# Performance work log

Hardware: AMD Instinct MI355X
Metric: run time of the kernel (lower is better)

## Reference

```python
import jax, jax.numpy as jnp
import numpy as np

N = 50000
E = 800000
DIM_IN = 128
DIM_H = 16
HEADS = 8
DIM_OUT = 16
NEG_SLOPE = 0.2


def setup_inputs() -> dict:
    key = jax.random.key(0)
    ks = jax.random.split(key, 12)
    def glorot(k, shape):
        fan_in = shape[0]
        return jax.random.normal(k, shape, dtype=jnp.float32) / np.sqrt(fan_in)
    x = jax.random.normal(ks[0], (N, DIM_IN), dtype=jnp.float32)
    edge_index = jax.random.randint(ks[1], (2, E), 0, N, dtype=jnp.int64)
    # layer 1: GATv2Conv(dim_in, dim_h, heads=8)
    Wl1 = glorot(ks[2], (DIM_IN, HEADS * DIM_H))
    Wr1 = glorot(ks[3], (DIM_IN, HEADS * DIM_H))
    att1 = glorot(ks[4], (HEADS, DIM_H))
    bias1 = jnp.zeros((HEADS * DIM_H,), dtype=jnp.float32)
    # layer 2: GATv2Conv(dim_h*heads, dim_out, heads=1)
    Wl2 = glorot(ks[5], (HEADS * DIM_H, DIM_OUT))
    Wr2 = glorot(ks[6], (HEADS * DIM_H, DIM_OUT))
    att2 = glorot(ks[7], (1, DIM_OUT))
    bias2 = jnp.zeros((DIM_OUT,), dtype=jnp.float32)
    return {"x": x, "edge_index": edge_index, "Wl1": Wl1, "Wr1": Wr1,
            "att1": att1, "bias1": bias1, "Wl2": Wl2, "Wr2": Wr2,
            "att2": att2, "bias2": bias2}


def gatv2_layer(x, src, dst, Wl, Wr, att, bias, n_nodes, heads, ch):
    # x: [N, F_in]; src/dst: [Etot] (self-loops included)
    xl = (x @ Wl).reshape(n_nodes, heads, ch)  # source transform
    xr = (x @ Wr).reshape(n_nodes, heads, ch)  # target transform
    e = jax.nn.leaky_relu(xl[src] + xr[dst], NEG_SLOPE)      # [Etot, H, C]
    logits = jnp.einsum('ehc,hc->eh', e, att)                # [Etot, H]
    # segment softmax over incoming edges of each target node
    m = jax.ops.segment_max(logits, dst, num_segments=n_nodes)
    a = jnp.exp(logits - m[dst])
    denom = jax.ops.segment_sum(a, dst, num_segments=n_nodes)
    alpha = a / denom[dst]                                   # [Etot, H]
    out = jax.ops.segment_sum(xl[src] * alpha[:, :, None], dst,
                              num_segments=n_nodes)          # [N, H, C]
    return out.reshape(n_nodes, heads * ch) + bias


def reference(x, edge_index, Wl1, Wr1, att1, bias1, Wl2, Wr2, att2, bias2):
    # PyG GATv2Conv adds self-loops by default
    loops = jnp.arange(N, dtype=edge_index.dtype)
    src = jnp.concatenate([edge_index[0], loops])
    dst = jnp.concatenate([edge_index[1], loops])
    # dropout is identity in eval mode
    h = gatv2_layer(x, src, dst, Wl1, Wr1, att1, bias1, N, HEADS, DIM_H)
    h = jax.nn.elu(h)
    h = gatv2_layer(h, src, dst, Wl2, Wr2, att2, bias2, N, 1, DIM_OUT)
    return h, jax.nn.log_softmax(h, axis=1)
```

## Files before the change

kernel.cpp:

```cpp
#include <hip/hip_runtime.h>
#include <hip/hip_bf16.h>
#include <math.h>

#define NN 50000
#define EE 800000
#define DIN 128
#define HEADS 8
#define DH 16
#define DOUT 16
#define NEG 0.2f
#define GM 32
#define GB ((NN + GM - 1) / GM)
#define NB ((NN + 255) / 256)
#define ABLK ((EE / 4 + 255) / 256)
#define NPART 8
#define RANGE (NN / NPART)
#define RB 1563
#define SCATB 64
#define BUCKCAP 110000
#define PAD 64

typedef __attribute__((ext_vector_type(8))) short bf16x8;
typedef __attribute__((ext_vector_type(4))) float f32x4;
typedef __attribute__((ext_vector_type(4))) int i32x4;

__device__ __forceinline__ unsigned pack2bf(float a, float b) {
    union { __hip_bfloat162 h; unsigned u; } c;
    c.h = __float22bfloat162_rn(make_float2(a, b));
    return c.u;
}
__device__ __forceinline__ unsigned short f2bf(float v) {
    union { __hip_bfloat16 h; unsigned short u; } c;
    c.h = __float2bfloat16(v);
    return c.u;
}
__device__ __forceinline__ float bflo(unsigned u) { return __uint_as_float(u << 16); }
__device__ __forceinline__ float bfhi(unsigned u) { return __uint_as_float(u & 0xffff0000u); }

__global__ __launch_bounds__(256) void init_wcvt(int* __restrict__ cnt,
                                                 unsigned* __restrict__ bhead,
                                                 const float* __restrict__ Wl,
                                                 const float* __restrict__ Wr,
                                                 unsigned short* __restrict__ Wb,
                                                 const float* __restrict__ Wl2,
                                                 const float* __restrict__ Wr2,
                                                 unsigned short* __restrict__ Wb2) {
    int b = blockIdx.x, t = threadIdx.x;
    if (b == 0 && t < 8) bhead[t] = 0;
    if (b < NB) {
        int i = b * 256 + t;
        if (i < NN) cnt[i] = 1;
    } else if (b < NB + 128) {
        int i = (b - NB) * 256 + t;
        int n = i >> 7, k = i & 127;
        float v = (n < 128) ? Wl[k * 128 + n] : Wr[k * 128 + (n - 128)];
        Wb[i] = f2bf(v);
    } else {
        int i = (b - NB - 128) * 256 + t;
        int n = i >> 7, k = i & 127;
        float v = (n < 16) ? Wl2[k * 16 + n] : Wr2[k * 16 + (n - 16)];
        Wb2[i] = f2bf(v);
    }
}

__global__ __launch_bounds__(256) void fill_gemm1(const int* __restrict__ ei,
                                                  unsigned* __restrict__ bhead,
                                                  unsigned* __restrict__ bucket,
                                                  const float* __restrict__ x,
                                                  const unsigned short* __restrict__ Wb,
                                                  unsigned short* __restrict__ xlb,
                                                  float* __restrict__ xr) {
    __shared__ unsigned short As[GM][136];
    int t = threadIdx.x;
    if (blockIdx.x < ABLK) {
        unsigned* lrec = (unsigned*)&As[0][0];
        unsigned* lcnt = lrec + 1024;
        unsigned* loff = lcnt + 8;
        unsigned* lpos = loff + 8;
        unsigned* gbase = lpos + 8;
        int i = blockIdx.x * 256 + t;
        bool valid = i < EE / 4;
        i32x4 ss, dd;
        unsigned bb[4];
        if (valid) {
            ss = __builtin_nontemporal_load(((const i32x4*)ei) + i);
            dd = __builtin_nontemporal_load(((const i32x4*)(ei + EE)) + i);
        }
        if (t < 8) { lcnt[t] = 0; lpos[t] = 0; }
        __syncthreads();
        if (valid) {
#pragma unroll
            for (int e = 0; e < 4; ++e) {
                bb[e] = (unsigned)dd[e] / RANGE;
                atomicAdd(&lcnt[bb[e]], 1u);
            }
        }
        __syncthreads();
        if (t == 0) {
            unsigned run = 0;
#pragma unroll
            for (int q = 0; q < 8; ++q) { loff[q] = run; run += lcnt[q]; }
        }
        if (t < 8 && lcnt[t] > 0) gbase[t] = atomicAdd(&bhead[t], lcnt[t]);
        __syncthreads();
        if (valid) {
#pragma unroll
            for (int e = 0; e < 4; ++e) {
                unsigned p = atomicAdd(&lpos[bb[e]], 1u);
                lrec[loff[bb[e]] + p] = ((unsigned)ss[e] << 16) | (unsigned)dd[e];
            }
        }
        __syncthreads();
        unsigned total = loff[7] + lcnt[7];
        for (unsigned j = t; j < total; j += 256) {
            unsigned q = 0;
            while (q < 7 && j >= loff[q + 1]) ++q;
            bucket[(size_t)q * BUCKCAP + gbase[q] + (j - loff[q])] = lrec[j];
        }
        return;
    }
    int n0 = (blockIdx.x - ABLK) * GM;
    {
        int row = t >> 3, seg = t & 7;
        int nsrc = n0 + row < NN ? n0 + row : NN - 1;
        const f32x4* xp = (const f32x4*)(x + (size_t)nsrc * DIN + 16 * seg);
        f32x4 v0 = __builtin_nontemporal_load(xp);
        f32x4 v1 = __builtin_nontemporal_load(xp + 1);
        f32x4 v2 = __builtin_nontemporal_load(xp + 2);
        f32x4 v3 = __builtin_nontemporal_load(xp + 3);
        uint4 p0 = make_uint4(pack2bf(v0[0], v0[1]), pack2bf(v0[2], v0[3]),
                              pack2bf(v1[0], v1[1]), pack2bf(v1[2], v1[3]));
        uint4 p1 = make_uint4(pack2bf(v2[0], v2[1]), pack2bf(v2[2], v2[3]),
                              pack2bf(v3[0], v3[1]), pack2bf(v3[2], v3[3]));
        *(uint4*)&As[row][16 * seg]     = p0;
        *(uint4*)&As[row][16 * seg + 8] = p1;
    }
    __syncthreads();
    int lane = t & 63, w = t >> 6;
    int m = lane & 15, quad = lane >> 4;
    f32x4 acc[2][4];
#pragma unroll
    for (int mt = 0; mt < 2; ++mt)
#pragma unroll
        for (int nt = 0; nt < 4; ++nt) acc[mt][nt] = (f32x4){0.f, 0.f, 0.f, 0.f};
#pragma unroll
    for (int ks = 0; ks < 4; ++ks) {
        int k = 32 * ks + 8 * quad;
        bf16x8 a0 = *(const bf16x8*)&As[m][k];
        bf16x8 a1 = *(const bf16x8*)&As[16 + m][k];
#pragma unroll
        for (int nt = 0; nt < 4; ++nt) {
            int n = 64 * w + 16 * nt + m;
            bf16x8 b = *(const bf16x8*)(Wb + (size_t)n * 128 + k);
            acc[0][nt] = __builtin_amdgcn_mfma_f32_16x16x32_bf16(a0, b, acc[0][nt], 0, 0, 0);
            acc[1][nt] = __builtin_amdgcn_mfma_f32_16x16x32_bf16(a1, b, acc[1][nt], 0, 0, 0);
        }
    }
#pragma unroll
    for (int mt = 0; mt < 2; ++mt) {
#pragma unroll
        for (int nt = 0; nt < 4; ++nt) {
            int col = 64 * w + 16 * nt + m;
            int rbase = n0 + 16 * mt + 4 * quad;
            if (col < 128) {
#pragma unroll
                for (int r = 0; r < 4; ++r) {
                    int row = rbase + r;
                    if (row < NN) xlb[(size_t)row * DIN + col] = f2bf(acc[mt][nt][r]);
                }
            } else {
#pragma unroll
                for (int r = 0; r < 4; ++r) {
                    int row = rbase + r;
                    if (row < NN) xr[(size_t)row * DIN + (col - 128)] = acc[mt][nt][r];
                }
            }
        }
    }
}

__global__ __launch_bounds__(256) void scatter_b(const unsigned* __restrict__ bucket,
                                                 const unsigned* __restrict__ bhead,
                                                 int* __restrict__ cnt,
                                                 unsigned short* __restrict__ esrcPad) {
    int r = blockIdx.x & 7;
    int g = blockIdx.x >> 3;
    int t = threadIdx.x;
    if (g == 0) {
        for (int dq = t; dq < RANGE; dq += 256) {
            int d = r * RANGE + dq;
            esrcPad[(size_t)d * PAD] = (unsigned short)d;
        }
    }
    unsigned n = bhead[r];
    for (unsigned i = (unsigned)g * 256 + t; i < n; i += SCATB * 256) {
        unsigned rec = __builtin_nontemporal_load(bucket + (size_t)r * BUCKCAP + i);
        unsigned s = rec >> 16, d = rec & 0xffffu;
        int p = atomicAdd(&cnt[d], 1);
        esrcPad[(size_t)d * PAD + p] = (unsigned short)s;
    }
}

__global__ __launch_bounds__(256) void l1_fused(const unsigned short* __restrict__ esrcPad,
                                                const int* __restrict__ cnt,
                                                const unsigned short* __restrict__ xlb,
                                                const float* __restrict__ xr,
                                                const float* __restrict__ att,
                                                const float* __restrict__ bias,
                                                unsigned short* __restrict__ hb) {
    int r = blockIdx.x & 7;
    int dq = (blockIdx.x >> 3) * 4 + (threadIdx.x >> 6);
    if (dq >= RANGE) return;
    int d = r * RANGE + dq;
    int lane = threadIdx.x & 63;
    int quarter = lane >> 4;
    int q16 = lane & 15;
    int rs = d * PAD;
    int re = rs + cnt[d];
    int last = re - 1;
    float4 xr0 = ((const float4*)(xr + (size_t)d * DIN))[2 * q16];
    float4 xr1 = ((const float4*)(xr + (size_t)d * DIN))[2 * q16 + 1];
    float4 at0 = ((const float4*)att)[2 * q16];
    float4 at1 = ((const float4*)att)[2 * q16 + 1];
    float4 a0 = make_float4(0.f, 0.f, 0.f, 0.f);
    float4 a1 = make_float4(0.f, 0.f, 0.f, 0.f);
    float l = 0.f;
    int slot = rs + quarter;
    int c0 = slot < last ? slot : last;
    int s0 = esrcPad[c0];
    int c1 = slot + 4 < last ? slot + 4 : last;
    int s1 = esrcPad[c1];
    uint4 row = ((const uint4*)(xlb + (size_t)s0 * DIN))[q16];
    for (; slot < re; slot += 4) {
        uint4 cur = row;
        int c2 = slot + 8 < last ? slot + 8 : last;
        int s2 = esrcPad[c2];
        row = ((const uint4*)(xlb + (size_t)s1 * DIN))[q16];
        s1 = s2;
        float f0 = bflo(cur.x), f1 = bfhi(cur.x);
        float f2 = bflo(cur.y), f3 = bfhi(cur.y);
        float f4 = bflo(cur.z), f5 = bfhi(cur.z);
        float f6 = bflo(cur.w), f7 = bfhi(cur.w);
        float v0 = f0 + xr0.x; v0 = fmaxf(v0, NEG * v0);
        float v1 = f1 + xr0.y; v1 = fmaxf(v1, NEG * v1);
        float v2 = f2 + xr0.z; v2 = fmaxf(v2, NEG * v2);
        float v3 = f3 + xr0.w; v3 = fmaxf(v3, NEG * v3);
        float v4 = f4 + xr1.x; v4 = fmaxf(v4, NEG * v4);
        float v5 = f5 + xr1.y; v5 = fmaxf(v5, NEG * v5);
        float v6 = f6 + xr1.z; v6 = fmaxf(v6, NEG * v6);
        float v7 = f7 + xr1.w; v7 = fmaxf(v7, NEG * v7);
        float w = at0.x * v0 + at0.y * v1 + at0.z * v2 + at0.w * v3
                + at1.x * v4 + at1.y * v5 + at1.z * v6 + at1.w * v7;
        w += __shfl_xor(w, 1);
        float p = __expf(w);
        a0.x += p * f0; a0.y += p * f1; a0.z += p * f2; a0.w += p * f3;
        a1.x += p * f4; a1.y += p * f5; a1.z += p * f6; a1.w += p * f7;
        l += p;
    }
#pragma unroll
    for (int off = 16; off < 64; off <<= 1) {
        a0.x += __shfl_xor(a0.x, off); a0.y += __shfl_xor(a0.y, off);
        a0.z += __shfl_xor(a0.z, off); a0.w += __shfl_xor(a0.w, off);
        a1.x += __shfl_xor(a1.x, off); a1.y += __shfl_xor(a1.y, off);
        a1.z += __shfl_xor(a1.z, off); a1.w += __shfl_xor(a1.w, off);
        l += __shfl_xor(l, off);
    }
    if (quarter == 0) {
        float inv = 1.f / l;
        float4 b0 = ((const float4*)bias)[2 * q16];
        float4 b1 = ((const float4*)bias)[2 * q16 + 1];
        float4 o0, o1;
        o0.x = a0.x * inv + b0.x; o0.x = o0.x > 0.f ? o0.x : expm1f(o0.x);
        o0.y = a0.y * inv + b0.y; o0.y = o0.y > 0.f ? o0.y : expm1f(o0.y);
        o0.z = a0.z * inv + b0.z; o0.z = o0.z > 0.f ? o0.z : expm1f(o0.z);
        o0.w = a0.w * inv + b0.w; o0.w = o0.w > 0.f ? o0.w : expm1f(o0.w);
        o1.x = a1.x * inv + b1.x; o1.x = o1.x > 0.f ? o1.x : expm1f(o1.x);
        o1.y = a1.y * inv + b1.y; o1.y = o1.y > 0.f ? o1.y : expm1f(o1.y);
        o1.z = a1.z * inv + b1.z; o1.z = o1.z > 0.f ? o1.z : expm1f(o1.z);
        o1.w = a1.w * inv + b1.w; o1.w = o1.w > 0.f ? o1.w : expm1f(o1.w);
        uint4 pk = make_uint4(pack2bf(o0.x, o0.y), pack2bf(o0.z, o0.w),
                              pack2bf(o1.x, o1.y), pack2bf(o1.z, o1.w));
        ((uint4*)(hb + (size_t)d * DIN))[q16] = pk;
    }
}

__global__ __launch_bounds__(256) void gemm2(const unsigned short* __restrict__ hb,
                                             const unsigned short* __restrict__ Wb2,
                                             float* __restrict__ xl2, float* __restrict__ xr2) {
    __shared__ unsigned short As[GM][136];
    int t = threadIdx.x;
    int n0 = blockIdx.x * GM;
    {
        int row = t >> 3, s8 = t & 7;
        int nsrc = n0 + row < NN ? n0 + row : NN - 1;
        const uint4* src = (const uint4*)(hb + (size_t)nsrc * DIN);
        *(uint4*)&As[row][8 * s8]      = src[s8];
        *(uint4*)&As[row][8 * s8 + 64] = src[s8 + 8];
    }
    __syncthreads();
    int lane = t & 63, w = t >> 6;
    int m = lane & 15, quad = lane >> 4;
    int mt = w & 1, nt = w >> 1;
    f32x4 acc = (f32x4){0.f, 0.f, 0.f, 0.f};
#pragma unroll
    for (int ks = 0; ks < 4; ++ks) {
        int k = 32 * ks + 8 * quad;
        bf16x8 a = *(const bf16x8*)&As[16 * mt + m][k];
        bf16x8 b = *(const bf16x8*)(Wb2 + (size_t)(16 * nt + m) * 128 + k);
        acc = __builtin_amdgcn_mfma_f32_16x16x32_bf16(a, b, acc, 0, 0, 0);
    }
    float* __restrict__ dst = (nt == 0) ? xl2 : xr2;
#pragma unroll
    for (int r = 0; r < 4; ++r) {
        int node = n0 + 16 * mt + 4 * quad + r;
        if (node < NN) dst[(size_t)node * DOUT + m] = acc[r];
    }
}

__global__ __launch_bounds__(256) void l2_fused(const unsigned short* __restrict__ esrcPad,
                                                const int* __restrict__ cnt,
                                                const float* __restrict__ xl,
                                                const float* __restrict__ xr,
                                                const float* __restrict__ att,
                                                const float* __restrict__ bias,
                                                float* __restrict__ out) {
    int r = blockIdx.x & 7;
    int dq = (blockIdx.x >> 3) * 4 + (threadIdx.x >> 6);
    if (dq >= RANGE) return;
    int d = r * RANGE + dq;
    int lane = threadIdx.x & 63;
    int sl = lane >> 2;
    int q = lane & 3;
    int rs = d * PAD;
    int re = rs + cnt[d];
    int last = re - 1;
    float4 xrq = ((const float4*)(xr + (size_t)d * DOUT))[q];
    float4 atq = ((const float4*)att)[q];
    float4 acc = make_float4(0.f, 0.f, 0.f, 0.f);
    float l = 0.f;
    int slot = rs + sl;
    int c0 = slot < last ? slot : last;
    int s0 = esrcPad[c0];
    for (; slot < re; slot += 16) {
        int c1 = slot + 16 < last ? slot + 16 : last;
        int s1 = esrcPad[c1];
        float4 cur = ((const float4*)(xl + (size_t)s0 * DOUT))[q];
        s0 = s1;
        float v0 = cur.x + xrq.x; v0 = fmaxf(v0, NEG * v0);
        float v1 = cur.y + xrq.y; v1 = fmaxf(v1, NEG * v1);
        float v2 = cur.z + xrq.z; v2 = fmaxf(v2, NEG * v2);
        float v3 = cur.w + xrq.w; v3 = fmaxf(v3, NEG * v3);
        float w = atq.x * v0 + atq.y * v1 + atq.z * v2 + atq.w * v3;
        w += __shfl_xor(w, 1);
        w += __shfl_xor(w, 2);
        float p = __expf(w);
        acc.x += p * cur.x; acc.y += p * cur.y;
        acc.z += p * cur.z; acc.w += p * cur.w;
        l += p;
    }
#pragma unroll
    for (int off = 4; off < 64; off <<= 1) {
        acc.x += __shfl_xor(acc.x, off);
        acc.y += __shfl_xor(acc.y, off);
        acc.z += __shfl_xor(acc.z, off);
        acc.w += __shfl_xor(acc.w, off);
        l += __shfl_xor(l, off);
    }
    float inv = 1.f / l;
    float4 b = ((const float4*)bias)[q];
    float4 v;
    v.x = acc.x * inv + b.x; v.y = acc.y * inv + b.y;
    v.z = acc.z * inv + b.z; v.w = acc.w * inv + b.w;
    float m = fmaxf(fmaxf(v.x, v.y), fmaxf(v.z, v.w));
    m = fmaxf(m, __shfl_xor(m, 1));
    m = fmaxf(m, __shfl_xor(m, 2));
    float es = __expf(v.x - m) + __expf(v.y - m) + __expf(v.z - m) + __expf(v.w - m);
    es += __shfl_xor(es, 1);
    es += __shfl_xor(es, 2);
    float lse = m + __logf(es);
    if (sl == 0) {
        ((float4*)(out + (size_t)d * DOUT))[q] = v;
        float4 ls;
        ls.x = v.x - lse; ls.y = v.y - lse; ls.z = v.z - lse; ls.w = v.w - lse;
        ((float4*)(out + (size_t)NN * DOUT + (size_t)d * DOUT))[q] = ls;
    }
}

extern "C" void kernel_launch(void* const* d_in, const int* in_sizes, int n_in,
                              void* d_out, int out_size, void* d_ws, size_t ws_size,
                              hipStream_t stream) {
    const float* x     = (const float*)d_in[0];
    const int*   ei    = (const int*)d_in[1];
    const float* Wl1   = (const float*)d_in[2];
    const float* Wr1   = (const float*)d_in[3];
    const float* att1  = (const float*)d_in[4];
    const float* bias1 = (const float*)d_in[5];
    const float* Wl2   = (const float*)d_in[6];
    const float* Wr2   = (const float*)d_in[7];
    const float* att2  = (const float*)d_in[8];
    const float* bias2 = (const float*)d_in[9];
    float* out = (float*)d_out;

    float* xr1    = (float*)d_ws;
    float* xl2    = xr1 + (size_t)NN * DIN;
    float* xr2    = xl2 + (size_t)NN * DOUT;
    unsigned short* xlb = (unsigned short*)(xr2 + (size_t)NN * DOUT);
    unsigned short* hb  = xlb + (size_t)NN * DIN;
    unsigned short* Wb  = hb + (size_t)NN * DIN;
    unsigned short* Wb2 = Wb + 256 * 128;
    unsigned short* esrcPad = Wb2 + 32 * 128;
    int*   cnt    = (int*)(esrcPad + (size_t)NN * PAD);
    unsigned* bucket = (unsigned*)(cnt + NN);
    unsigned* bhead  = bucket + (size_t)8 * BUCKCAP;

    const int B = 256;
    init_wcvt<<<NB + 144, B, 0, stream>>>(cnt, bhead, Wl1, Wr1, Wb, Wl2, Wr2, Wb2);
    fill_gemm1<<<ABLK + GB, B, 0, stream>>>(ei, bhead, bucket, x, Wb, xlb, xr1);
    scatter_b<<<NPART * SCATB, B, 0, stream>>>(bucket, bhead, cnt, esrcPad);

    l1_fused<<<NPART * RB, B, 0, stream>>>(esrcPad, cnt, xlb, xr1, att1, bias1, hb);

    gemm2<<<GB, B, 0, stream>>>(hb, Wb2, xl2, xr2);

    l2_fused<<<NPART * RB, B, 0, stream>>>(esrcPad, cnt, xl2, xr2, att2, bias2, out);
}
```

Baseline: 237.2 us.

## Fuse layer-1 aggregation with gemm2 and regroup bucket, scatter and gemm1 kernels

The edge bucketing pass moves into the init kernel, with bhead zeroed by a memset. The CSR scatter now shares a launch with the layer-1 GEMM so the two independent phases can overlap. Layer-1 attention aggregation writes each block's 32 output rows into shared memory and runs the layer-2 MFMA GEMM there, which removes the bf16 hidden-feature buffer and its global write and read. In exchange, each wave processes 8 destination nodes one after another instead of one, and blocks at partition boundaries recompute a few nodes that belong to the next partition.

```diff
diff --git a/kernel.cpp b/kernel.cpp
--- a/kernel.cpp
+++ b/kernel.cpp
@@ -16,6 +16,7 @@
 #define NPART 8
 #define RANGE (NN / NPART)
 #define RB 1563
+#define L1B 196
 #define SCATB 64
 #define BUCKCAP 110000
 #define PAD 64
@@ -37,89 +38,107 @@
 __device__ __forceinline__ float bflo(unsigned u) { return __uint_as_float(u << 16); }
 __device__ __forceinline__ float bfhi(unsigned u) { return __uint_as_float(u & 0xffff0000u); }
 
-__global__ __launch_bounds__(256) void init_wcvt(int* __restrict__ cnt,
-                                                 unsigned* __restrict__ bhead,
-                                                 const float* __restrict__ Wl,
-                                                 const float* __restrict__ Wr,
-                                                 unsigned short* __restrict__ Wb,
-                                                 const float* __restrict__ Wl2,
-                                                 const float* __restrict__ Wr2,
-                                                 unsigned short* __restrict__ Wb2) {
+__global__ __launch_bounds__(256) void init_bucket(int* __restrict__ cnt,
+                                                   const float* __restrict__ Wl,
+                                                   const float* __restrict__ Wr,
+                                                   unsigned short* __restrict__ Wb,
+                                                   const float* __restrict__ Wl2,
+                                                   const float* __restrict__ Wr2,
+                                                   unsigned short* __restrict__ Wb2,
+                                                   const int* __restrict__ ei,
+                                                   unsigned* __restrict__ bhead,
+                                                   unsigned* __restrict__ bucket) {
     int b = blockIdx.x, t = threadIdx.x;
-    if (b == 0 && t < 8) bhead[t] = 0;
     if (b < NB) {
         int i = b * 256 + t;
         if (i < NN) cnt[i] = 1;
+        return;
     } else if (b < NB + 128) {
         int i = (b - NB) * 256 + t;
         int n = i >> 7, k = i & 127;
         float v = (n < 128) ? Wl[k * 128 + n] : Wr[k * 128 + (n - 128)];
         Wb[i] = f2bf(v);
-    } else {
+        return;
+    } else if (b < NB + 144) {
         int i = (b - NB - 128) * 256 + t;
         int n = i >> 7, k = i & 127;
         float v = (n < 16) ? Wl2[k * 16 + n] : Wr2[k * 16 + (n - 16)];
         Wb2[i] = f2bf(v);
-    }
-}
-
-__global__ __launch_bounds__(256) void fill_gemm1(const int* __restrict__ ei,
-                                                  unsigned* __restrict__ bhead,
-                                                  unsigned* __restrict__ bucket,
+        return;
+    }
+    __shared__ unsigned lrec[1024];
+    __shared__ unsigned lcnt[8], loff[8], lpos[8], gbase[8];
+    int ab = b - (NB + 144);
+    int i = ab * 256 + t;
+    bool valid = i < EE / 4;
+    i32x4 ss, dd;
+    unsigned bb[4];
+    if (valid) {
+        ss = __builtin_nontemporal_load(((const i32x4*)ei) + i);
+        dd = __builtin_nontemporal_load(((const i32x4*)(ei + EE)) + i);
+    }
+    if (t < 8) { lcnt[t] = 0; lpos[t] = 0; }
+    __syncthreads();
+    if (valid) {
+#pragma unroll
+        for (int e = 0; e < 4; ++e) {
+            bb[e] = (unsigned)dd[e] / RANGE;
+            atomicAdd(&lcnt[bb[e]], 1u);
+        }
+    }
+    __syncthreads();
+    if (t == 0) {
+        unsigned run = 0;
+#pragma unroll
+        for (int q = 0; q < 8; ++q) { loff[q] = run; run += lcnt[q]; }
+    }
+    if (t < 8 && lcnt[t] > 0) gbase[t] = atomicAdd(&bhead[t], lcnt[t]);
+    __syncthreads();
+    if (valid) {
+#pragma unroll
+        for (int e = 0; e < 4; ++e) {
+            unsigned p = atomicAdd(&lpos[bb[e]], 1u);
+            lrec[loff[bb[e]] + p] = ((unsigned)ss[e] << 16) | (unsigned)dd[e];
+        }
+    }
+    __syncthreads();
+    unsigned total = loff[7] + lcnt[7];
+    for (unsigned j = t; j < total; j += 256) {
+        unsigned q = 0;
+        while (q < 7 && j >= loff[q + 1]) ++q;
+        bucket[(size_t)q * BUCKCAP + gbase[q] + (j - loff[q])] = lrec[j];
+    }
+}
+
+__global__ __launch_bounds__(256) void scat_gemm1(const unsigned* __restrict__ bucket,
+                                                  const unsigned* __restrict__ bhead,
+                                                  int* __restrict__ cnt,
+                                                  unsigned short* __restrict__ esrcPad,
                                                   const float* __restrict__ x,
                                                   const unsigned short* __restrict__ Wb,
                                                   unsigned short* __restrict__ xlb,
                                                   float* __restrict__ xr) {
     __shared__ unsigned short As[GM][136];
     int t = threadIdx.x;
-    if (blockIdx.x < ABLK) {
-        unsigned* lrec = (unsigned*)&As[0][0];
-        unsigned* lcnt = lrec + 1024;
-        unsigned* loff = lcnt + 8;
-        unsigned* lpos = loff + 8;
-        unsigned* gbase = lpos + 8;
-        int i = blockIdx.x * 256 + t;
-        bool valid = i < EE / 4;
-        i32x4 ss, dd;
-        unsigned bb[4];
-        if (valid) {
-            ss = __builtin_nontemporal_load(((const i32x4*)ei) + i);
-            dd = __builtin_nontemporal_load(((const i32x4*)(ei + EE)) + i);
-        }
-        if (t < 8) { lcnt[t] = 0; lpos[t] = 0; }
-        __syncthreads();
-        if (valid) {
-#pragma unroll
-            for (int e = 0; e < 4; ++e) {
-                bb[e] = (unsigned)dd[e] / RANGE;
-                atomicAdd(&lcnt[bb[e]], 1u);
+    if (blockIdx.x < NPART * SCATB) {
+        int r = blockIdx.x & 7;
+        int g = blockIdx.x >> 3;
+        if (g == 0) {
+            for (int dq = t; dq < RANGE; dq += 256) {
+                int d = r * RANGE + dq;
+                esrcPad[(size_t)d * PAD] = (unsigned short)d;
             }
         }
-        __syncthreads();
-        if (t == 0) {
-            unsigned run = 0;
-#pragma unroll
-            for (int q = 0; q < 8; ++q) { loff[q] = run; run += lcnt[q]; }
-        }
-        if (t < 8 && lcnt[t] > 0) gbase[t] = atomicAdd(&bhead[t], lcnt[t]);
-        __syncthreads();
-        if (valid) {
-#pragma unroll
-            for (int e = 0; e < 4; ++e) {
-                unsigned p = atomicAdd(&lpos[bb[e]], 1u);
-                lrec[loff[bb[e]] + p] = ((unsigned)ss[e] << 16) | (unsigned)dd[e];
-            }
-        }
-        __syncthreads();
-        unsigned total = loff[7] + lcnt[7];
-        for (unsigned j = t; j < total; j += 256) {
-            unsigned q = 0;
-            while (q < 7 && j >= loff[q + 1]) ++q;
-            bucket[(size_t)q * BUCKCAP + gbase[q] + (j - loff[q])] = lrec[j];
+        unsigned n = bhead[r];
+        for (unsigned i = (unsigned)g * 256 + t; i < n; i += SCATB * 256) {
+            unsigned rec = __builtin_nontemporal_load(bucket + (size_t)r * BUCKCAP + i);
+            unsigned s = rec >> 16, d = rec & 0xffffu;
+            int p = atomicAdd(&cnt[d], 1);
+            esrcPad[(size_t)d * PAD + p] = (unsigned short)s;
         }
         return;
     }
-    int n0 = (blockIdx.x - ABLK) * GM;
+    int n0 = (blockIdx.x - NPART * SCATB) * GM;
     {
         int row = t >> 3, seg = t & 7;
         int nsrc = n0 + row < NN ? n0 + row : NN - 1;
@@ -179,128 +198,99 @@
     }
 }
 
-__global__ __launch_bounds__(256) void scatter_b(const unsigned* __restrict__ bucket,
-                                                 const unsigned* __restrict__ bhead,
-                                                 int* __restrict__ cnt,
-                                                 unsigned short* __restrict__ esrcPad) {
-    int r = blockIdx.x & 7;
-    int g = blockIdx.x >> 3;
-    int t = threadIdx.x;
-    if (g == 0) {
-        for (int dq = t; dq < RANGE; dq += 256) {
-            int d = r * RANGE + dq;
-            esrcPad[(size_t)d * PAD] = (unsigned short)d;
-        }
-    }
-    unsigned n = bhead[r];
-    for (unsigned i = (unsigned)g * 256 + t; i < n; i += SCATB * 256) {
-        unsigned rec = __builtin_nontemporal_load(bucket + (size_t)r * BUCKCAP + i);
-        unsigned s = rec >> 16, d = rec & 0xffffu;
-        int p = atomicAdd(&cnt[d], 1);
-        esrcPad[(size_t)d * PAD + p] = (unsigned short)s;
-    }
-}
-
-__global__ __launch_bounds__(256) void l1_fused(const unsigned short* __restrict__ esrcPad,
+__global__ __launch_bounds__(256) void l1_gemm2(const unsigned short* __restrict__ esrcPad,
                                                 const int* __restrict__ cnt,
                                                 const unsigned short* __restrict__ xlb,
                                                 const float* __restrict__ xr,
                                                 const float* __restrict__ att,
                                                 const float* __restrict__ bias,
-                                                unsigned short* __restrict__ hb) {
+                                                const unsigned short* __restrict__ Wb2,
+                                                float* __restrict__ xl2,
+                                                float* __restrict__ xr2) {
+    __shared__ unsigned short As[GM][136];
     int r = blockIdx.x & 7;
-    int dq = (blockIdx.x >> 3) * 4 + (threadIdx.x >> 6);
-    if (dq >= RANGE) return;
-    int d = r * RANGE + dq;
-    int lane = threadIdx.x & 63;
+    int gbase0 = r * RANGE + (blockIdx.x >> 3) * GM;
+    int t = threadIdx.x;
+    int lane = t & 63, wv = t >> 6;
     int quarter = lane >> 4;
     int q16 = lane & 15;
-    int rs = d * PAD;
-    int re = rs + cnt[d];
-    int last = re - 1;
-    float4 xr0 = ((const float4*)(xr + (size_t)d * DIN))[2 * q16];
-    float4 xr1 = ((const float4*)(xr + (size_t)d * DIN))[2 * q16 + 1];
     float4 at0 = ((const float4*)att)[2 * q16];
     float4 at1 = ((const float4*)att)[2 * q16 + 1];
-    float4 a0 = make_float4(0.f, 0.f, 0.f, 0.f);
-    float4 a1 = make_float4(0.f, 0.f, 0.f, 0.f);
-    float l = 0.f;
-    int slot = rs + quarter;
-    int c0 = slot < last ? slot : last;
-    int s0 = esrcPad[c0];
-    int c1 = slot + 4 < last ? slot + 4 : last;
-    int s1 = esrcPad[c1];
-    uint4 row = ((const uint4*)(xlb + (size_t)s0 * DIN))[q16];
-    for (; slot < re; slot += 4) {
-        uint4 cur = row;
-        int c2 = slot + 8 < last ? slot + 8 : last;
-        int s2 = esrcPad[c2];
-        row = ((const uint4*)(xlb + (size_t)s1 * DIN))[q16];
-        s1 = s2;
-        float f0 = bflo(cur.x), f1 = bfhi(cur.x);
-        float f2 = bflo(cur.y), f3 = bfhi(cur.y);
-        float f4 = bflo(cur.z), f5 = bfhi(cur.z);
-        float f6 = bflo(cur.w), f7 = bfhi(cur.w);
-        float v0 = f0 + xr0.x; v0 = fmaxf(v0, NEG * v0);
-        float v1 = f1 + xr0.y; v1 = fmaxf(v1, NEG * v1);
-        float v2 = f2 + xr0.z; v2 = fmaxf(v2, NEG * v2);
-        float v3 = f3 + xr0.w; v3 = fmaxf(v3, NEG * v3);
-        float v4 = f4 + xr1.x; v4 = fmaxf(v4, NEG * v4);
-        float v5 = f5 + xr1.y; v5 = fmaxf(v5, NEG * v5);
-        float v6 = f6 + xr1.z; v6 = fmaxf(v6, NEG * v6);
-        float v7 = f7 + xr1.w; v7 = fmaxf(v7, NEG * v7);
-        float w = at0.x * v0 + at0.y * v1 + at0.z * v2 + at0.w * v3
-                + at1.x * v4 + at1.y * v5 + at1.z * v6 + at1.w * v7;
-        w += __shfl_xor(w, 1);
-        float p = __expf(w);
-        a0.x += p * f0; a0.y += p * f1; a0.z += p * f2; a0.w += p * f3;
-        a1.x += p * f4; a1.y += p * f5; a1.z += p * f6; a1.w += p * f7;
-        l += p;
-    }
-#pragma unroll
-    for (int off = 16; off < 64; off <<= 1) {
-        a0.x += __shfl_xor(a0.x, off); a0.y += __shfl_xor(a0.y, off);
-        a0.z += __shfl_xor(a0.z, off); a0.w += __shfl_xor(a0.w, off);
-        a1.x += __shfl_xor(a1.x, off); a1.y += __shfl_xor(a1.y, off);
-        a1.z += __shfl_xor(a1.z, off); a1.w += __shfl_xor(a1.w, off);
-        l += __shfl_xor(l, off);
-    }
-    if (quarter == 0) {
-        float inv = 1.f / l;
-        float4 b0 = ((const float4*)bias)[2 * q16];
-        float4 b1 = ((const float4*)bias)[2 * q16 + 1];
-        float4 o0, o1;
-        o0.x = a0.x * inv + b0.x; o0.x = o0.x > 0.f ? o0.x : expm1f(o0.x);
-        o0.y = a0.y * inv + b0.y; o0.y = o0.y > 0.f ? o0.y : expm1f(o0.y);
-        o0.z = a0.z * inv + b0.z; o0.z = o0.z > 0.f ? o0.z : expm1f(o0.z);
-        o0.w = a0.w * inv + b0.w; o0.w = o0.w > 0.f ? o0.w : expm1f(o0.w);
-        o1.x = a1.x * inv + b1.x; o1.x = o1.x > 0.f ? o1.x : expm1f(o1.x);
-        o1.y = a1.y * inv + b1.y; o1.y = o1.y > 0.f ? o1.y : expm1f(o1.y);
-        o1.z = a1.z * inv + b1.z; o1.z = o1.z > 0.f ? o1.z : expm1f(o1.z);
-        o1.w = a1.w * inv + b1.w; o1.w = o1.w > 0.f ? o1.w : expm1f(o1.w);
-        uint4 pk = make_uint4(pack2bf(o0.x, o0.y), pack2bf(o0.z, o0.w),
-                              pack2bf(o1.x, o1.y), pack2bf(o1.z, o1.w));
-        ((uint4*)(hb + (size_t)d * DIN))[q16] = pk;
-    }
-}
-
-__global__ __launch_bounds__(256) void gemm2(const unsigned short* __restrict__ hb,
-                                             const unsigned short* __restrict__ Wb2,
-                                             float* __restrict__ xl2, float* __restrict__ xr2) {
-    __shared__ unsigned short As[GM][136];
-    int t = threadIdx.x;
-    int n0 = blockIdx.x * GM;
-    {
-        int row = t >> 3, s8 = t & 7;
-        int nsrc = n0 + row < NN ? n0 + row : NN - 1;
-        const uint4* src = (const uint4*)(hb + (size_t)nsrc * DIN);
-        *(uint4*)&As[row][8 * s8]      = src[s8];
-        *(uint4*)&As[row][8 * s8 + 64] = src[s8 + 8];
-    }
-    __syncthreads();
-    int lane = t & 63, w = t >> 6;
+    float4 b0 = ((const float4*)bias)[2 * q16];
+    float4 b1 = ((const float4*)bias)[2 * q16 + 1];
+#pragma unroll 1
+    for (int j = 0; j < 8; ++j) {
+        int lrow = wv * 8 + j;
+        int d = gbase0 + lrow;
+        if (d < NN) {
+            int rs = d * PAD;
+            int re = rs + cnt[d];
+            int last = re - 1;
+            float4 xr0 = ((const float4*)(xr + (size_t)d * DIN))[2 * q16];
+            float4 xr1 = ((const float4*)(xr + (size_t)d * DIN))[2 * q16 + 1];
+            float4 a0 = make_float4(0.f, 0.f, 0.f, 0.f);
+            float4 a1 = make_float4(0.f, 0.f, 0.f, 0.f);
+            float l = 0.f;
+            int slot = rs + quarter;
+            int c0 = slot < last ? slot : last;
+            int s0 = esrcPad[c0];
+            int c1 = slot + 4 < last ? slot + 4 : last;
+            int s1 = esrcPad[c1];
+            uint4 row = ((const uint4*)(xlb + (size_t)s0 * DIN))[q16];
+            for (; slot < re; slot += 4) {
+                uint4 cur = row;
+                int c2 = slot + 8 < last ? slot + 8 : last;
+                int s2 = esrcPad[c2];
+                row = ((const uint4*)(xlb + (size_t)s1 * DIN))[q16];
+                s1 = s2;
+                float f0 = bflo(cur.x), f1 = bfhi(cur.x);
+                float f2 = bflo(cur.y), f3 = bfhi(cur.y);
+                float f4 = bflo(cur.z), f5 = bfhi(cur.z);
+                float f6 = bflo(cur.w), f7 = bfhi(cur.w);
+                float v0 = f0 + xr0.x; v0 = fmaxf(v0, NEG * v0);
+                float v1 = f1 + xr0.y; v1 = fmaxf(v1, NEG * v1);
+                float v2 = f2 + xr0.z; v2 = fmaxf(v2, NEG * v2);
+                float v3 = f3 + xr0.w; v3 = fmaxf(v3, NEG * v3);
+                float v4 = f4 + xr1.x; v4 = fmaxf(v4, NEG * v4);
+                float v5 = f5 + xr1.y; v5 = fmaxf(v5, NEG * v5);
+                float v6 = f6 + xr1.z; v6 = fmaxf(v6, NEG * v6);
+                float v7 = f7 + xr1.w; v7 = fmaxf(v7, NEG * v7);
+                float w = at0.x * v0 + at0.y * v1 + at0.z * v2 + at0.w * v3
+                        + at1.x * v4 + at1.y * v5 + at1.z * v6 + at1.w * v7;
+                w += __shfl_xor(w, 1);
+                float p = __expf(w);
+                a0.x += p * f0; a0.y += p * f1; a0.z += p * f2; a0.w += p * f3;
+                a1.x += p * f4; a1.y += p * f5; a1.z += p * f6; a1.w += p * f7;
+                l += p;
+            }
+#pragma unroll
+            for (int off = 16; off < 64; off <<= 1) {
+                a0.x += __shfl_xor(a0.x, off); a0.y += __shfl_xor(a0.y, off);
+                a0.z += __shfl_xor(a0.z, off); a0.w += __shfl_xor(a0.w, off);
+                a1.x += __shfl_xor(a1.x, off); a1.y += __shfl_xor(a1.y, off);
+                a1.z += __shfl_xor(a1.z, off); a1.w += __shfl_xor(a1.w, off);
+                l += __shfl_xor(l, off);
+            }
+            if (quarter == 0) {
+                float inv = 1.f / l;
+                float4 o0, o1;
+                o0.x = a0.x * inv + b0.x; o0.x = o0.x > 0.f ? o0.x : expm1f(o0.x);
+                o0.y = a0.y * inv + b0.y; o0.y = o0.y > 0.f ? o0.y : expm1f(o0.y);
+                o0.z = a0.z * inv + b0.z; o0.z = o0.z > 0.f ? o0.z : expm1f(o0.z);
+                o0.w = a0.w * inv + b0.w; o0.w = o0.w > 0.f ? o0.w : expm1f(o0.w);
+                o1.x = a1.x * inv + b1.x; o1.x = o1.x > 0.f ? o1.x : expm1f(o1.x);
+                o1.y = a1.y * inv + b1.y; o1.y = o1.y > 0.f ? o1.y : expm1f(o1.y);
+                o1.z = a1.z * inv + b1.z; o1.z = o1.z > 0.f ? o1.z : expm1f(o1.z);
+                o1.w = a1.w * inv + b1.w; o1.w = o1.w > 0.f ? o1.w : expm1f(o1.w);
+                uint4 pk = make_uint4(pack2bf(o0.x, o0.y), pack2bf(o0.z, o0.w),
+                                      pack2bf(o1.x, o1.y), pack2bf(o1.z, o1.w));
+                *(uint4*)&As[lrow][8 * q16] = pk;
+            }
+        }
+    }
+    __syncthreads();
     int m = lane & 15, quad = lane >> 4;
-    int mt = w & 1, nt = w >> 1;
+    int mt = wv & 1, nt = wv >> 1;
     f32x4 acc = (f32x4){0.f, 0.f, 0.f, 0.f};
 #pragma unroll
     for (int ks = 0; ks < 4; ++ks) {
@@ -311,9 +301,9 @@
     }
     float* __restrict__ dst = (nt == 0) ? xl2 : xr2;
 #pragma unroll
-    for (int r = 0; r < 4; ++r) {
-        int node = n0 + 16 * mt + 4 * quad + r;
-        if (node < NN) dst[(size_t)node * DOUT + m] = acc[r];
+    for (int rr = 0; rr < 4; ++rr) {
+        int node = gbase0 + 16 * mt + 4 * quad + rr;
+        if (node < NN) dst[(size_t)node * DOUT + m] = acc[rr];
     }
 }
 
@@ -405,8 +395,7 @@
     float* xl2    = xr1 + (size_t)NN * DIN;
     float* xr2    = xl2 + (size_t)NN * DOUT;
     unsigned short* xlb = (unsigned short*)(xr2 + (size_t)NN * DOUT);
-    unsigned short* hb  = xlb + (size_t)NN * DIN;
-    unsigned short* Wb  = hb + (size_t)NN * DIN;
+    unsigned short* Wb  = xlb + (size_t)NN * DIN;
     unsigned short* Wb2 = Wb + 256 * 128;
     unsigned short* esrcPad = Wb2 + 32 * 128;
     int*   cnt    = (int*)(esrcPad + (size_t)NN * PAD);
@@ -414,13 +403,12 @@
     unsigned* bhead  = bucket + (size_t)8 * BUCKCAP;
 
     const int B = 256;
-    init_wcvt<<<NB + 144, B, 0, stream>>>(cnt, bhead, Wl1, Wr1, Wb, Wl2, Wr2, Wb2);
-    fill_gemm1<<<ABLK + GB, B, 0, stream>>>(ei, bhead, bucket, x, Wb, xlb, xr1);
-    scatter_b<<<NPART * SCATB, B, 0, stream>>>(bucket, bhead, cnt, esrcPad);
-
-    l1_fused<<<NPART * RB, B, 0, stream>>>(esrcPad, cnt, xlb, xr1, att1, bias1, hb);
-
-    gemm2<<<GB, B, 0, stream>>>(hb, Wb2, xl2, xr2);
-
+    hipMemsetAsync(bhead, 0, 8 * sizeof(unsigned), stream);
+    init_bucket<<<NB + 144 + ABLK, B, 0, stream>>>(cnt, Wl1, Wr1, Wb, Wl2, Wr2, Wb2,
+                                                   ei, bhead, bucket);
+    scat_gemm1<<<NPART * SCATB + GB, B, 0, stream>>>(bucket, bhead, cnt, esrcPad,
+                                                     x, Wb, xlb, xr1);
+    l1_gemm2<<<NPART * L1B, B, 0, stream>>>(esrcPad, cnt, xlb, xr1, att1, bias1,
+                                            Wb2, xl2, xr2);
     l2_fused<<<NPART * RB, B, 0, stream>>>(esrcPad, cnt, xl2, xr2, att2, bias2, out);
 }
```

Result: slower. 259.2 us (+9.3%).

## Regroup prep kernels: bucket fill with init, scatter with first GEMM

Applied to the files above, without the earlier changes.

The edge-bucketing pass moves out of the GEMM1 kernel into the init/weight-conversion kernel. The scatter-into-padded-adjacency pass is merged with GEMM1, so the stage boundaries are rearranged and the sequence keeps one fewer kernel launch. The bhead reset now uses a memset, because it must finish before the bucketing blocks start within the same launch. ELU also switches from expm1f to __expf(x)-1, which is cheaper but less accurate near zero.

```diff
diff --git a/kernel.cpp b/kernel.cpp
--- a/kernel.cpp
+++ b/kernel.cpp
@@ -36,90 +36,109 @@
 }
 __device__ __forceinline__ float bflo(unsigned u) { return __uint_as_float(u << 16); }
 __device__ __forceinline__ float bfhi(unsigned u) { return __uint_as_float(u & 0xffff0000u); }
-
-__global__ __launch_bounds__(256) void init_wcvt(int* __restrict__ cnt,
-                                                 unsigned* __restrict__ bhead,
-                                                 const float* __restrict__ Wl,
-                                                 const float* __restrict__ Wr,
-                                                 unsigned short* __restrict__ Wb,
-                                                 const float* __restrict__ Wl2,
-                                                 const float* __restrict__ Wr2,
-                                                 unsigned short* __restrict__ Wb2) {
+__device__ __forceinline__ float elu1(float x) { return x > 0.f ? x : __expf(x) - 1.f; }
+
+__global__ __launch_bounds__(256) void init_bucket(int* __restrict__ cnt,
+                                                   const float* __restrict__ Wl,
+                                                   const float* __restrict__ Wr,
+                                                   unsigned short* __restrict__ Wb,
+                                                   const float* __restrict__ Wl2,
+                                                   const float* __restrict__ Wr2,
+                                                   unsigned short* __restrict__ Wb2,
+                                                   const int* __restrict__ ei,
+                                                   unsigned* __restrict__ bhead,
+                                                   unsigned* __restrict__ bucket) {
     int b = blockIdx.x, t = threadIdx.x;
-    if (b == 0 && t < 8) bhead[t] = 0;
     if (b < NB) {
         int i = b * 256 + t;
         if (i < NN) cnt[i] = 1;
+        return;
     } else if (b < NB + 128) {
         int i = (b - NB) * 256 + t;
         int n = i >> 7, k = i & 127;
         float v = (n < 128) ? Wl[k * 128 + n] : Wr[k * 128 + (n - 128)];
         Wb[i] = f2bf(v);
-    } else {
+        return;
+    } else if (b < NB + 144) {
         int i = (b - NB - 128) * 256 + t;
         int n = i >> 7, k = i & 127;
         float v = (n < 16) ? Wl2[k * 16 + n] : Wr2[k * 16 + (n - 16)];
         Wb2[i] = f2bf(v);
-    }
-}
-
-__global__ __launch_bounds__(256) void fill_gemm1(const int* __restrict__ ei,
-                                                  unsigned* __restrict__ bhead,
-                                                  unsigned* __restrict__ bucket,
+        return;
+    }
+    __shared__ unsigned lrec[1024];
+    __shared__ unsigned lcnt[8], loff[8], lpos[8], gbase[8];
+    int ab = b - (NB + 144);
+    int i = ab * 256 + t;
+    bool valid = i < EE / 4;
+    i32x4 ss, dd;
+    unsigned bb[4];
+    if (valid) {
+        ss = __builtin_nontemporal_load(((const i32x4*)ei) + i);
+        dd = __builtin_nontemporal_load(((const i32x4*)(ei + EE)) + i);
+    }
+    if (t < 8) { lcnt[t] = 0; lpos[t] = 0; }
+    __syncthreads();
+    if (valid) {
+#pragma unroll
+        for (int e = 0; e < 4; ++e) {
+            bb[e] = (unsigned)dd[e] / RANGE;
+            atomicAdd(&lcnt[bb[e]], 1u);
+        }
+    }
+    __syncthreads();
+    if (t == 0) {
+        unsigned run = 0;
+#pragma unroll
+        for (int q = 0; q < 8; ++q) { loff[q] = run; run += lcnt[q]; }
+    }
+    if (t < 8 && lcnt[t] > 0) gbase[t] = atomicAdd(&bhead[t], lcnt[t]);
+    __syncthreads();
+    if (valid) {
+#pragma unroll
+        for (int e = 0; e < 4; ++e) {
+            unsigned p = atomicAdd(&lpos[bb[e]], 1u);
+            lrec[loff[bb[e]] + p] = ((unsigned)ss[e] << 16) | (unsigned)dd[e];
+        }
+    }
+    __syncthreads();
+    unsigned total = loff[7] + lcnt[7];
+    for (unsigned j = t; j < total; j += 256) {
+        unsigned q = 0;
+        while (q < 7 && j >= loff[q + 1]) ++q;
+        bucket[(size_t)q * BUCKCAP + gbase[q] + (j - loff[q])] = lrec[j];
+    }
+}
+
+__global__ __launch_bounds__(256) void scat_gemm1(const unsigned* __restrict__ bucket,
+                                                  const unsigned* __restrict__ bhead,
+                                                  int* __restrict__ cnt,
+                                                  unsigned short* __restrict__ esrcPad,
                                                   const float* __restrict__ x,
                                                   const unsigned short* __restrict__ Wb,
                                                   unsigned short* __restrict__ xlb,
                                                   float* __restrict__ xr) {
     __shared__ unsigned short As[GM][136];
     int t = threadIdx.x;
-    if (blockIdx.x < ABLK) {
-        unsigned* lrec = (unsigned*)&As[0][0];
-        unsigned* lcnt = lrec + 1024;
-        unsigned* loff = lcnt + 8;
-        unsigned* lpos = loff + 8;
-        unsigned* gbase = lpos + 8;
-        int i = blockIdx.x * 256 + t;
-        bool valid = i < EE / 4;
-        i32x4 ss, dd;
-        unsigned bb[4];
-        if (valid) {
-            ss = __builtin_nontemporal_load(((const i32x4*)ei) + i);
-            dd = __builtin_nontemporal_load(((const i32x4*)(ei + EE)) + i);
-        }
-        if (t < 8) { lcnt[t] = 0; lpos[t] = 0; }
-        __syncthreads();
-        if (valid) {
-#pragma unroll
-            for (int e = 0; e < 4; ++e) {
-                bb[e] = (unsigned)dd[e] / RANGE;
-                atomicAdd(&lcnt[bb[e]], 1u);
+    if (blockIdx.x < NPART * SCATB) {
+        int r = blockIdx.x & 7;
+        int g = blockIdx.x >> 3;
+        if (g == 0) {
+            for (int dq = t; dq < RANGE; dq += 256) {
+                int d = r * RANGE + dq;
+                esrcPad[(size_t)d * PAD] = (unsigned short)d;
             }
         }
-        __syncthreads();
-        if (t == 0) {
-            unsigned run = 0;
-#pragma unroll
-            for (int q = 0; q < 8; ++q) { loff[q] = run; run += lcnt[q]; }
-        }
-        if (t < 8 && lcnt[t] > 0) gbase[t] = atomicAdd(&bhead[t], lcnt[t]);
-        __syncthreads();
-        if (valid) {
-#pragma unroll
-            for (int e = 0; e < 4; ++e) {
-                unsigned p = atomicAdd(&lpos[bb[e]], 1u);
-                lrec[loff[bb[e]] + p] = ((unsigned)ss[e] << 16) | (unsigned)dd[e];
-            }
-        }
-        __syncthreads();
-        unsigned total = loff[7] + lcnt[7];
-        for (unsigned j = t; j < total; j += 256) {
-            unsigned q = 0;
-            while (q < 7 && j >= loff[q + 1]) ++q;
-            bucket[(size_t)q * BUCKCAP + gbase[q] + (j - loff[q])] = lrec[j];
+        unsigned n = bhead[r];
+        for (unsigned i = (unsigned)g * 256 + t; i < n; i += SCATB * 256) {
+            unsigned rec = __builtin_nontemporal_load(bucket + (size_t)r * BUCKCAP + i);
+            unsigned s = rec >> 16, d = rec & 0xffffu;
+            int p = atomicAdd(&cnt[d], 1);
+            esrcPad[(size_t)d * PAD + p] = (unsigned short)s;
         }
         return;
     }
-    int n0 = (blockIdx.x - ABLK) * GM;
+    int n0 = (blockIdx.x - NPART * SCATB) * GM;
     {
         int row = t >> 3, seg = t & 7;
         int nsrc = n0 + row < NN ? n0 + row : NN - 1;
@@ -176,28 +195,6 @@
                 }
             }
         }
-    }
-}
-
-__global__ __launch_bounds__(256) void scatter_b(const unsigned* __restrict__ bucket,
-                                                 const unsigned* __restrict__ bhead,
-                                                 int* __restrict__ cnt,
-                                                 unsigned short* __restrict__ esrcPad) {
-    int r = blockIdx.x & 7;
-    int g = blockIdx.x >> 3;
-    int t = threadIdx.x;
-    if (g == 0) {
-        for (int dq = t; dq < RANGE; dq += 256) {
-            int d = r * RANGE + dq;
-            esrcPad[(size_t)d * PAD] = (unsigned short)d;
-        }
-    }
-    unsigned n = bhead[r];
-    for (unsigned i = (unsigned)g * 256 + t; i < n; i += SCATB * 256) {
-        unsigned rec = __builtin_nontemporal_load(bucket + (size_t)r * BUCKCAP + i);
-        unsigned s = rec >> 16, d = rec & 0xffffu;
-        int p = atomicAdd(&cnt[d], 1);
-        esrcPad[(size_t)d * PAD + p] = (unsigned short)s;
     }
 }
 
@@ -270,14 +267,14 @@
         float4 b0 = ((const float4*)bias)[2 * q16];
         float4 b1 = ((const float4*)bias)[2 * q16 + 1];
         float4 o0, o1;
-        o0.x = a0.x * inv + b0.x; o0.x = o0.x > 0.f ? o0.x : expm1f(o0.x);
-        o0.y = a0.y * inv + b0.y; o0.y = o0.y > 0.f ? o0.y : expm1f(o0.y);
-        o0.z = a0.z * inv + b0.z; o0.z = o0.z > 0.f ? o0.z : expm1f(o0.z);
-        o0.w = a0.w * inv + b0.w; o0.w = o0.w > 0.f ? o0.w : expm1f(o0.w);
-        o1.x = a1.x * inv + b1.x; o1.x = o1.x > 0.f ? o1.x : expm1f(o1.x);
-        o1.y = a1.y * inv + b1.y; o1.y = o1.y > 0.f ? o1.y : expm1f(o1.y);
-        o1.z = a1.z * inv + b1.z; o1.z = o1.z > 0.f ? o1.z : expm1f(o1.z);
-        o1.w = a1.w * inv + b1.w; o1.w = o1.w > 0.f ? o1.w : expm1f(o1.w);
+        o0.x = elu1(a0.x * inv + b0.x);
+        o0.y = elu1(a0.y * inv + b0.y);
+        o0.z = elu1(a0.z * inv + b0.z);
+        o0.w = elu1(a0.w * inv + b0.w);
+        o1.x = elu1(a1.x * inv + b1.x);
+        o1.y = elu1(a1.y * inv + b1.y);
+        o1.z = elu1(a1.z * inv + b1.z);
+        o1.w = elu1(a1.w * inv + b1.w);
         uint4 pk = make_uint4(pack2bf(o0.x, o0.y), pack2bf(o0.z, o0.w),
                               pack2bf(o1.x, o1.y), pack2bf(o1.z, o1.w));
         ((uint4*)(hb + (size_t)d * DIN))[q16] = pk;
@@ -414,13 +411,12 @@
     unsigned* bhead  = bucket + (size_t)8 * BUCKCAP;
 
     const int B = 256;
-    init_wcvt<<<NB + 144, B, 0, stream>>>(cnt, bhead, Wl1, Wr1, Wb, Wl2, Wr2, Wb2);
-    fill_gemm1<<<ABLK + GB, B, 0, stream>>>(ei, bhead, bucket, x, Wb, xlb, xr1);
-    scatter_b<<<NPART * SCATB, B, 0, stream>>>(bucket, bhead, cnt, esrcPad);
-
+    hipMemsetAsync(bhead, 0, 8 * sizeof(unsigned), stream);
+    init_bucket<<<NB + 144 + ABLK, B, 0, stream>>>(cnt, Wl1, Wr1, Wb, Wl2, Wr2, Wb2,
+                                                   ei, bhead, bucket);
+    scat_gemm1<<<NPART * SCATB + GB, B, 0, stream>>>(bucket, bhead, cnt, esrcPad,
+                                                     x, Wb, xlb, xr1);
     l1_fused<<<NPART * RB, B, 0, stream>>>(esrcPad, cnt, xlb, xr1, att1, bias1, hb);
-
     gemm2<<<GB, B, 0, stream>>>(hb, Wb2, xl2, xr2);
-
     l2_fused<<<NPART * RB, B, 0, stream>>>(esrcPad, cnt, xl2, xr2, att2, bias2, out);
 }
```

New measurement: 228.0 us. 1.04x faster.
